# Kernel tuning notes

Hardware: AMD Instinct MI355X
Metric: run time of the kernel (lower is better)

Reference implementation:

```python
import jax, jax.numpy as jnp
import numpy as np

B, T, C = 4, 2048, 768
H, D = 12, 64          # num_heads, head_size
R = 64                 # kv_lora_rank
ROPE_THETA = 10000.0


def setup_inputs() -> dict:
    key = jax.random.key(0)
    ks = jax.random.split(key, 8)
    s = lambda fan_in: 1.0 / np.sqrt(fan_in)
    return {
        "x":      jax.random.normal(ks[0], (B, T, C), jnp.float32),
        "Wq":     jax.random.normal(ks[1], (C, H * D), jnp.float32) * s(C),
        "Wdown":  jax.random.normal(ks[2], (C, R), jnp.float32) * s(C),
        "ln_g":   jnp.ones((R,), jnp.float32),
        "ln_b":   jnp.zeros((R,), jnp.float32),
        "Wup":    jax.random.normal(ks[3], (R, 2 * H * D), jnp.float32) * s(R),
        "Wo":     jax.random.normal(ks[4], (H * D, C), jnp.float32) * s(H * D),
        "bo":     jnp.zeros((C,), jnp.float32),
    }


def _rope_cos_sin(t, d, dtype):
    # freqs over half-dim, repeated twice (rotate-half convention)
    inv_freq = 1.0 / (ROPE_THETA ** (jnp.arange(0, d, 2, dtype=jnp.float32) / d))
    ang = jnp.arange(t, dtype=jnp.float32)[:, None] * inv_freq[None, :]  # [T, D/2]
    ang = jnp.concatenate([ang, ang], axis=-1)                            # [T, D]
    return jnp.cos(ang).astype(dtype), jnp.sin(ang).astype(dtype)


def _apply_rope(q, cos, sin):
    # q: [B, H, T, D]; cos/sin: [T, D]
    d2 = q.shape[-1] // 2
    rot = jnp.concatenate([-q[..., d2:], q[..., :d2]], axis=-1)
    return q * cos + rot * sin


def reference(x, Wq, Wdown, ln_g, ln_b, Wup, Wo, bo):
    b, t, c = x.shape
    q = (x @ Wq).reshape(b, t, H, D).transpose(0, 2, 1, 3)  # [B,H,T,D]

    ckv = x @ Wdown                                         # [B,T,R]
    mu = jnp.mean(ckv, axis=-1, keepdims=True)
    var = jnp.var(ckv, axis=-1, keepdims=True)
    ckv = (ckv - mu) * jax.lax.rsqrt(var + 1e-5) * ln_g + ln_b

    kv = (ckv @ Wup).reshape(b, t, 2, H, D)
    k = kv[:, :, 0].transpose(0, 2, 1, 3)                   # [B,H,T,D]
    v = kv[:, :, 1].transpose(0, 2, 1, 3)

    cos, sin = _rope_cos_sin(t, D, x.dtype)
    q = _apply_rope(q, cos, sin)
    k = _apply_rope(k, cos, sin)

    wei = jnp.einsum("bhqd,bhkd->bhqk", q, k) * (D ** -0.5)
    causal = jnp.tril(jnp.ones((t, t), bool))
    wei = jnp.where(causal, wei, -jnp.inf)
    wei = jax.nn.softmax(wei, axis=-1)                      # dropout: eval mode (identity)

    out = jnp.einsum("bhqk,bhkd->bhqd", wei, v)             # [B,H,T,D]
    out = out.transpose(0, 2, 1, 3).reshape(b, t, H * D)
    return out @ Wo + bo
```

## Files before the change

### kernel.cpp

```cpp
#include <hip/hip_runtime.h>
#include <hip/hip_bf16.h>
#include <math.h>

#define B_ 4
#define T_ 2048
#define C_ 768
#define H_ 12
#define D_ 64
#define R_ 64
#define BT_ (B_*T_)
#define HD_ (H_*D_)

typedef __attribute__((ext_vector_type(8))) short bf16x8;
typedef __attribute__((ext_vector_type(4))) float f32x4;
typedef __attribute__((ext_vector_type(16))) float f32x16;

__device__ inline short f2bf(float f) {
  union { float f; unsigned u; } x; x.f = f;
  unsigned r = x.u + 0x7fffu + ((x.u >> 16) & 1u);
  return (short)(r >> 16);
}
__device__ inline unsigned pk_bf16(float a, float b) {
#if __has_builtin(__builtin_amdgcn_cvt_pk_bf16_f32)
  auto t = __builtin_amdgcn_cvt_pk_bf16_f32(a, b);
  unsigned u; __builtin_memcpy(&u, &t, sizeof(unsigned)); return u;
#else
  union { float f; unsigned u; } x, y; x.f = a; y.f = b;
  unsigned ra = (x.u + 0x7fffu + ((x.u >> 16) & 1u)) >> 16;
  unsigned rb = (y.u + 0x7fffu + ((y.u >> 16) & 1u)) & 0xffff0000u;
  return ra | rb;
#endif
}
__device__ inline float fexp2(float x) {
#if __has_builtin(__builtin_amdgcn_exp2f)
  return __builtin_amdgcn_exp2f(x);
#else
  return exp2f(x);
#endif
}
__device__ inline void pswap(unsigned &a, unsigned &b) {
#if __has_builtin(__builtin_amdgcn_permlane32_swap)
  auto r = __builtin_amdgcn_permlane32_swap((int)a, (int)b, false, false);
  unsigned u[2]; __builtin_memcpy(u, &r, 8);
  a = u[0]; b = u[1];
#else
  unsigned ax = __shfl_xor(a, 32), bx = __shfl_xor(b, 32);
  bool hi = (threadIdx.x & 32) != 0;
  unsigned na = hi ? bx : a;
  unsigned nb = hi ? b : ax;
  a = na; b = nb;
#endif
}
typedef __attribute__((address_space(3))) unsigned lds_u32;
typedef __attribute__((address_space(1))) const unsigned glb_u32;
__device__ inline void gload_lds16(const void* g, void* l) {
  __builtin_amdgcn_global_load_lds((glb_u32*)g, (lds_u32*)l, 16, 0, 0);
}

__device__ inline void ttile(const float* __restrict__ src, short* __restrict__ dst,
                             int K, int N, int k0, int n0, int tid, float (*tl)[33]) {
  int tx = tid & 31, ty = tid >> 5;
  #pragma unroll
  for (int r = 0; r < 4; ++r)
    tl[ty + 8 * r][tx] = src[(size_t)(k0 + ty + 8 * r) * N + n0 + tx];
  __syncthreads();
  #pragma unroll
  for (int r = 0; r < 4; ++r)
    dst[(size_t)(n0 + ty + 8 * r) * K + k0 + tx] = f2bf(tl[tx][ty + 8 * r]);
}

#define NCONV (BT_*C_/4/256)

__global__ __launch_bounds__(256) void prep_conv(
    const float* __restrict__ x, short* __restrict__ x_bf,
    const float* __restrict__ Wq, const float* __restrict__ Wd,
    const float* __restrict__ Wup, const float* __restrict__ Wo,
    short* __restrict__ W1T, short* __restrict__ WupT, short* __restrict__ WoT,
    float* __restrict__ cs, float* __restrict__ sn) {
  __shared__ float tl[32][33];
  int tid = threadIdx.x;
  if (blockIdx.x < NCONV) {
    int i = blockIdx.x * 256 + tid;
    float4 v = ((const float4*)x)[i];
    short4 o;
    o.x = f2bf(v.x); o.y = f2bf(v.y); o.z = f2bf(v.z); o.w = f2bf(v.w);
    ((short4*)x_bf)[i] = o;
    return;
  }
  int blk = blockIdx.x - NCONV;
  if (blk < 576) {
    int tk = blk % 24, tn = blk / 24;
    ttile(Wq, W1T, 768, 768, tk * 32, tn * 32, tid, tl);
  } else if (blk < 624) {
    int l = blk - 576; int tk = l % 24, tn = l / 24;
    ttile(Wd, W1T + (size_t)768 * 768, 768, 64, tk * 32, tn * 32, tid, tl);
  } else if (blk < 720) {
    int l = blk - 624; int tk = l % 2, tn = l / 2;
    ttile(Wup, WupT, 64, 1536, tk * 32, tn * 32, tid, tl);
  } else if (blk < 1296) {
    int l = blk - 720; int tk = l % 24, tn = l / 24;
    ttile(Wo, WoT, 768, 768, tk * 32, tn * 32, tid, tl);
  } else {
    int base = (blk - 1296) * 1024;
    #pragma unroll
    for (int i = 0; i < 4; ++i) {
      int idx = base + tid + i * 256;
      int j = idx & 31, t = idx >> 5;
      float invf = exp2f(-(float)j * (13.287712379549449f / 32.f));
      float a = (float)t * invf;
      cs[idx] = cosf(a);
      sn[idx] = sinf(a);
    }
  }
}

#define SC2_ 0.18033688f

template<int MODE>
__global__ __launch_bounds__(256) void gemm128(
    const short* __restrict__ A, const short* __restrict__ Bt,
    int M, int N, int K,
    float* __restrict__ out0, const float* __restrict__ bias,
    const float* __restrict__ bias2,
    short* __restrict__ ob0, short* __restrict__ ob1,
    const float* __restrict__ cs, const float* __restrict__ sn)
{
  __shared__ short SM[2 * 128 * 64];
  short* As = SM;
  short* Bs = SM + 128 * 64;
  const int m0 = blockIdx.x * 128;
  const int n0 = blockIdx.y * 128;
  const int tid = threadIdx.x, lane = tid & 63, w = tid >> 6;
  const int wr = w >> 1, wc = w & 1;
  const int fr = lane & 15, fk = (lane >> 4) * 8;
  const int rstage = lane >> 3;
  const int cstage = (lane & 7) * 8;

  f32x4 acc[4][4] = {};

  for (int k0 = 0; k0 < K; k0 += 64) {
    __syncthreads();
    #pragma unroll
    for (int i = 0; i < 4; ++i) {
      int c = w * 4 + i;
      int r = c * 8 + rstage;
      gload_lds16(&A[(size_t)(m0 + r) * K + k0 + cstage], &As[c * 512]);
      gload_lds16(&Bt[(size_t)(n0 + r) * K + k0 + cstage], &Bs[c * 512]);
    }
    __syncthreads();
    #pragma unroll
    for (int kk = 0; kk < 64; kk += 32) {
      bf16x8 a[4], b[4];
      #pragma unroll
      for (int mi = 0; mi < 4; ++mi)
        a[mi] = *(const bf16x8*)&As[(wr * 64 + mi * 16 + fr) * 64 + kk + fk];
      #pragma unroll
      for (int ni = 0; ni < 4; ++ni)
        b[ni] = *(const bf16x8*)&Bs[(wc * 64 + ni * 16 + fr) * 64 + kk + fk];
      #pragma unroll
      for (int mi = 0; mi < 4; ++mi)
        #pragma unroll
        for (int ni = 0; ni < 4; ++ni)
          acc[mi][ni] = __builtin_amdgcn_mfma_f32_16x16x32_bf16(a[mi], b[ni], acc[mi][ni], 0, 0, 0);
    }
  }

  const int er = (lane >> 4) * 4, ec = lane & 15;
  const int cb = n0 + wc * 64;

  if (cb < 768) {
    int h = cb >> 6;
    #pragma unroll
    for (int mi = 0; mi < 4; ++mi)
      #pragma unroll
      for (int r = 0; r < 4; ++r) {
        int row = m0 + wr * 64 + mi * 16 + er + r;
        int t = row & (T_ - 1), bb = row >> 11;
        short* dst = ob0 + (((size_t)(bb * H_ + h)) * T_ + t) * 64;
        #pragma unroll
        for (int ni = 0; ni < 2; ++ni) {
          int d = ni * 16 + ec;
          float c = cs[t * 32 + d], s = sn[t * 32 + d];
          if constexpr (MODE == 0) { c *= SC2_; s *= SC2_; }
          float x0 = acc[mi][ni][r], x1 = acc[mi][ni + 2][r];
          dst[d]      = f2bf(x0 * c - x1 * s);
          dst[d + 32] = f2bf(x1 * c + x0 * s);
        }
      }
  } else if constexpr (MODE == 0) {
    if (cb == 768) {
      #pragma unroll
      for (int mi = 0; mi < 4; ++mi)
        #pragma unroll
        for (int r = 0; r < 4; ++r) {
          float s = 0.f, s2 = 0.f;
          #pragma unroll
          for (int ni = 0; ni < 4; ++ni) { float v = acc[mi][ni][r]; s += v; s2 += v*v; }
          #pragma unroll
          for (int off = 1; off < 16; off <<= 1) {
            s  += __shfl_xor(s, off);
            s2 += __shfl_xor(s2, off);
          }
          float mu = s * (1.f/64.f);
          float var = s2 * (1.f/64.f) - mu * mu;
          float rstd = rsqrtf(var + 1e-5f);
          int row = m0 + wr * 64 + mi * 16 + er + r;
          #pragma unroll
          for (int ni = 0; ni < 4; ++ni) {
            int d = ni * 16 + ec;
            ob1[(size_t)row * 64 + d] = f2bf((acc[mi][ni][r] - mu) * rstd * bias[d] + bias2[d]);
          }
        }
    }
  } else {
    __syncthreads();
    short* Wl = SM + w * 2560;
    int h = (cb - 768) >> 6;
    int bb = m0 >> 11;
    int dl = lane >> 2, tl = (lane & 3) * 8;
    #pragma unroll
    for (int hp = 0; hp < 2; ++hp) {
      #pragma unroll
      for (int mi2 = 0; mi2 < 2; ++mi2) {
        int mi = hp * 2 + mi2;
        int tl0 = mi2 * 16 + er;
        #pragma unroll
        for (int ni = 0; ni < 4; ++ni) {
          int d = ni * 16 + ec;
          uint2 uu;
          uu.x = pk_bf16(acc[mi][ni][0], acc[mi][ni][1]);
          uu.y = pk_bf16(acc[mi][ni][2], acc[mi][ni][3]);
          *(uint2*)&Wl[d * 40 + tl0] = uu;
        }
      }
      int tg0 = (m0 & (T_ - 1)) + wr * 64 + hp * 32;
      #pragma unroll
      for (int j = 0; j < 4; ++j) {
        int d = j * 16 + dl;
        uint4 vv = *(const uint4*)&Wl[d * 40 + tl];
        *(uint4*)&ob1[((size_t)(bb * H_ + h) * 64 + d) * T_ + tg0 + tl] = vv;
      }
    }
  }
}

template<int MODE>
__global__ __launch_bounds__(256) void gemm64(
    const short* __restrict__ A, const short* __restrict__ Bt,
    int M, int N, int K,
    float* __restrict__ out0, const float* __restrict__ bias,
    const float* __restrict__ bias2,
    short* __restrict__ ob0, short* __restrict__ ob1,
    const float* __restrict__ cs, const float* __restrict__ sn)
{
  __shared__ short SM[128 * 64 + 64 * 64];
  short* As = SM;
  short* Bs = SM + 128 * 64;
  const int m0 = blockIdx.x * 128;
  const int n0 = blockIdx.y * 64;
  const int tid = threadIdx.x, lane = tid & 63, w = tid >> 6;
  const int fr = lane & 15, fk = (lane >> 4) * 8;
  const int rstage = lane >> 3;
  const int cstage = (lane & 7) * 8;

  f32x4 acc[2][4] = {};

  for (int k0 = 0; k0 < K; k0 += 64) {
    __syncthreads();
    #pragma unroll
    for (int i = 0; i < 4; ++i) {
      int c = w * 4 + i;
      int r = c * 8 + rstage;
      gload_lds16(&A[(size_t)(m0 + r) * K + k0 + cstage], &As[c * 512]);
    }
    #pragma unroll
    for (int i = 0; i < 2; ++i) {
      int c = w * 2 + i;
      int r = c * 8 + rstage;
      gload_lds16(&Bt[(size_t)(n0 + r) * K + k0 + cstage], &Bs[c * 512]);
    }
    __syncthreads();
    #pragma unroll
    for (int kk = 0; kk < 64; kk += 32) {
      bf16x8 a[2], b[4];
      a[0] = *(const bf16x8*)&As[(w * 32 +      fr) * 64 + kk + fk];
      a[1] = *(const bf16x8*)&As[(w * 32 + 16 + fr) * 64 + kk + fk];
      #pragma unroll
      for (int ni = 0; ni < 4; ++ni)
        b[ni] = *(const bf16x8*)&Bs[(ni * 16 + fr) * 64 + kk + fk];
      #pragma unroll
      for (int mi = 0; mi < 2; ++mi)
        #pragma unroll
        for (int ni = 0; ni < 4; ++ni)
          acc[mi][ni] = __builtin_amdgcn_mfma_f32_16x16x32_bf16(a[mi], b[ni], acc[mi][ni], 0, 0, 0);
    }
  }

  const int er = (lane >> 4) * 4, ec = lane & 15;

  if constexpr (MODE == 2) {
    #pragma unroll
    for (int mi = 0; mi < 2; ++mi)
      #pragma unroll
      for (int r = 0; r < 4; ++r) {
        int row = m0 + w * 32 + mi * 16 + er + r;
        #pragma unroll
        for (int ni = 0; ni < 4; ++ni) {
          int col = n0 + ni * 16 + ec;
          out0[(size_t)row * N + col] = acc[mi][ni][r] + bias[col];
        }
      }
    return;
  }
}

__global__ __launch_bounds__(256) void attn_mfma(
    const short* __restrict__ qgl, const short* __restrict__ kg,
    const short* __restrict__ vtg, short* __restrict__ o)
{
  __shared__ short SMa[2][2][8 * 512];

  const int bh = blockIdx.x;
  const int u  = 15 - blockIdx.y;
  const int tid = threadIdx.x, lane = tid & 63, w = tid >> 6;
  const int q32 = lane & 31, half = lane >> 5;
  const short* kb  = kg  + (size_t)bh * T_ * 64;
  const short* vtb = vtg + (size_t)bh * 64 * T_;
  const int b = bh / H_, h = bh - b * H_;

  const int wq = 4 * u + w;
  const int q0 = wq * 32;
  const int last_w = (wq >> 1) * 64;
  const int qidx = q0 + q32;
  const int kend = (2 * u + 1) * 64;

  const short* qrow = qgl + ((size_t)bh * T_ + qidx) * 64;
  bf16x8 bq[4];
  #pragma unroll
  for (int ks = 0; ks < 4; ++ks)
    bq[ks] = *(const bf16x8*)&qrow[ks * 16 + half * 8];

  f32x16 oacc[2] = {};
  float lrun = 0.f;

  auto stage = [&](int buf, int kt) {
    #pragma unroll
    for (int i = 0; i < 2; ++i) {
      int c = w * 2 + i;
      int kh = c >> 2, ks = c & 3;
      gload_lds16(kb + (size_t)(kt + kh * 32 + q32) * 64 + ks * 16 + half * 8,
                  &SMa[buf][0][c * 512]);
      gload_lds16(vtb + (size_t)(kh * 32 + q32) * T_ + kt + ks * 16 + half * 8,
                  &SMa[buf][1][c * 512]);
    }
  };

  stage(0, 0);
  __syncthreads();

  int cur = 0;
  for (int kt = 0; kt <= kend; kt += 64) {
    if (kt + 64 <= kend) stage(cur ^ 1, kt + 64);

    if (kt <= last_w) {
      const short* Kc = &SMa[cur][0][0];
      const short* Vc = &SMa[cur][1][0];
      const bool diag = (kt == last_w);
      const int dkh = diag ? (wq & 1) : 2;
      const bool skip1 = diag && ((wq & 1) == 0);

      bf16x8 bp[4];
      #pragma unroll
      for (int kh = 0; kh < 2; ++kh) {
        if (kh == 1 && skip1) break;
        f32x16 sacc = {};
        __builtin_amdgcn_s_setprio(1);
        #pragma unroll
        for (int ks = 0; ks < 4; ++ks) {
          bf16x8 a = *(const bf16x8*)&Kc[(kh * 4 + ks) * 512 + lane * 8];
          sacc = __builtin_amdgcn_mfma_f32_32x32x16_bf16(a, bq[ks], sacc, 0, 0, 0);
        }
        __builtin_amdgcn_s_setprio(0);
        float pv[16];
        if (kh != dkh) {
          #pragma unroll
          for (int r = 0; r < 16; ++r) pv[r] = fexp2(sacc[r]);
        } else {
          #pragma unroll
          for (int r = 0; r < 16; ++r) {
            int key = kt + kh * 32 + (r & 3) + 8 * (r >> 2) + 4 * half;
            pv[r] = (key <= qidx) ? fexp2(sacc[r]) : 0.f;
          }
        }
        float t0 = (pv[0] + pv[1]) + (pv[2] + pv[3]);
        float t1 = (pv[4] + pv[5]) + (pv[6] + pv[7]);
        float t2 = (pv[8] + pv[9]) + (pv[10] + pv[11]);
        float t3 = (pv[12] + pv[13]) + (pv[14] + pv[15]);
        lrun += (t0 + t1) + (t2 + t3);
        unsigned l0 = pk_bf16(pv[0],  pv[1]),  h0 = pk_bf16(pv[2],  pv[3]);
        unsigned l1 = pk_bf16(pv[4],  pv[5]),  h1 = pk_bf16(pv[6],  pv[7]);
        unsigned l2 = pk_bf16(pv[8],  pv[9]),  h2 = pk_bf16(pv[10], pv[11]);
        unsigned l3 = pk_bf16(pv[12], pv[13]), h3 = pk_bf16(pv[14], pv[15]);
        pswap(l0, l1); pswap(h0, h1);
        pswap(l2, l3); pswap(h2, h3);
        union { unsigned u[4]; bf16x8 v; } f0, f1;
        f0.u[0] = l0; f0.u[1] = h0; f0.u[2] = l1; f0.u[3] = h1;
        f1.u[0] = l2; f1.u[1] = h2; f1.u[2] = l3; f1.u[3] = h3;
        bp[2 * kh + 0] = f0.v;
        bp[2 * kh + 1] = f1.v;
      }

      __builtin_amdgcn_s_setprio(1);
      #pragma unroll
      for (int ks = 0; ks < 2; ++ks)
        #pragma unroll
        for (int dt = 0; dt < 2; ++dt) {
          bf16x8 av = *(const bf16x8*)&Vc[(dt * 4 + ks) * 512 + lane * 8];
          oacc[dt] = __builtin_amdgcn_mfma_f32_32x32x16_bf16(av, bp[ks], oacc[dt], 0, 0, 0);
        }
      if (!skip1) {
        #pragma unroll
        for (int ks = 2; ks < 4; ++ks)
          #pragma unroll
          for (int dt = 0; dt < 2; ++dt) {
            bf16x8 av = *(const bf16x8*)&Vc[(dt * 4 + ks) * 512 + lane * 8];
            oacc[dt] = __builtin_amdgcn_mfma_f32_32x32x16_bf16(av, bp[ks], oacc[dt], 0, 0, 0);
          }
      }
      __builtin_amdgcn_s_setprio(0);
    }

    __syncthreads();
    cur ^= 1;
  }

  float ltot = lrun + __shfl_xor(lrun, 32);
  float inv = 1.f / ltot;
  short* Pw = &SMa[0][0][0] + w * 2304;
  #pragma unroll
  for (int dt = 0; dt < 2; ++dt)
    #pragma unroll
    for (int g2 = 0; g2 < 4; ++g2) {
      uint2 uu;
      uu.x = pk_bf16(oacc[dt][4 * g2 + 0] * inv, oacc[dt][4 * g2 + 1] * inv);
      uu.y = pk_bf16(oacc[dt][4 * g2 + 2] * inv, oacc[dt][4 * g2 + 3] * inv);
      *(uint2*)&Pw[q32 * 72 + dt * 32 + 8 * g2 + 4 * half] = uu;
    }
  int row = lane >> 1, seg = lane & 1;
  int t = q0 + row;
  short* orow = o + ((size_t)(b * T_ + t)) * HD_ + h * 64 + seg * 32;
  #pragma unroll
  for (int i = 0; i < 4; ++i) {
    uint4 vv = *(const uint4*)&Pw[row * 72 + seg * 32 + i * 8];
    *(uint4*)&orow[i * 8] = vv;
  }
}

extern "C" void kernel_launch(void* const* d_in, const int* in_sizes, int n_in,
                              void* d_out, int out_size, void* d_ws, size_t ws_size,
                              hipStream_t stream) {
  (void)in_sizes; (void)n_in; (void)out_size; (void)ws_size;
  const float* x     = (const float*)d_in[0];
  const float* Wq    = (const float*)d_in[1];
  const float* Wdown = (const float*)d_in[2];
  const float* ln_g  = (const float*)d_in[3];
  const float* ln_b  = (const float*)d_in[4];
  const float* Wup   = (const float*)d_in[5];
  const float* Wo    = (const float*)d_in[6];
  const float* bo    = (const float*)d_in[7];
  float* out = (float*)d_out;

  char* w = (char*)d_ws;
  short* x_bf   = (short*)w;  w += (size_t)BT_ * C_    * 2;
  short* W1T    = (short*)w;  w += (size_t)896 * C_    * 2;
  short* WupT   = (short*)w;  w += (size_t)2*HD_ * R_  * 2;
  short* WoT    = (short*)w;  w += (size_t)HD_ * C_    * 2;
  short* ckv    = (short*)w;  w += (size_t)BT_ * R_    * 2;
  short* qb     = (short*)w;  w += (size_t)BT_ * HD_   * 2;
  short* kb     = (short*)w;  w += (size_t)BT_ * HD_   * 2;
  short* vt     = (short*)w;  w += (size_t)BT_ * HD_   * 2;
  short* att    = (short*)w;  w += (size_t)BT_ * HD_   * 2;
  float* cs_t   = (float*)w;  w += (size_t)T_ * 32 * 4;
  float* sn_t   = (float*)w;  w += (size_t)T_ * 32 * 4;

  prep_conv<<<NCONV + 1360, 256, 0, stream>>>(x, x_bf, Wq, Wdown, Wup, Wo,
                                              W1T, WupT, WoT, cs_t, sn_t);

  gemm128<0><<<dim3(BT_/128, 7), 256, 0, stream>>>(
      x_bf, W1T, BT_, 832, C_, nullptr, ln_g, ln_b, qb, ckv, cs_t, sn_t);

  gemm128<1><<<dim3(BT_/128, 12), 256, 0, stream>>>(
      ckv, WupT, BT_, 2*HD_, R_, nullptr, nullptr, nullptr, kb, vt, cs_t, sn_t);

  attn_mfma<<<dim3(B_*H_, 16), 256, 0, stream>>>(qb, kb, vt, att);

  gemm64<2><<<dim3(BT_/128, 12), 256, 0, stream>>>(
      att, WoT, BT_, C_, HD_, out, bo, nullptr, nullptr, nullptr, nullptr, nullptr);
}
```

Measured before the change: 193.1 us.

## Fuse x fp32-to-bf16 conversion into QKV GEMM and double-buffer GEMM K loops

Removes the separate x→bf16 conversion pass from the prep kernel. The first projection GEMM now loads fp32 x directly into registers, converts it, and writes it to LDS. That GEMM and the output-projection GEMM both get double-buffered LDS, so the next K tile loads while the current one computes. This saves a full write and read of a bf16 copy of x and hides load latency, at the cost of twice the LDS per block (64KB for gemm128 MODE0). That may lower occupancy. The latent-up GEMM (K=64) is simplified to a single stage.

New measurement: 194.4 us. About the same (+0.7%).

```diff
diff --git a/kernel.cpp b/kernel.cpp
--- a/kernel.cpp
+++ b/kernel.cpp
@@ -69,25 +69,14 @@
     dst[(size_t)(n0 + ty + 8 * r) * K + k0 + tx] = f2bf(tl[tx][ty + 8 * r]);
 }
 
-#define NCONV (BT_*C_/4/256)
-
 __global__ __launch_bounds__(256) void prep_conv(
-    const float* __restrict__ x, short* __restrict__ x_bf,
     const float* __restrict__ Wq, const float* __restrict__ Wd,
     const float* __restrict__ Wup, const float* __restrict__ Wo,
     short* __restrict__ W1T, short* __restrict__ WupT, short* __restrict__ WoT,
     float* __restrict__ cs, float* __restrict__ sn) {
   __shared__ float tl[32][33];
   int tid = threadIdx.x;
-  if (blockIdx.x < NCONV) {
-    int i = blockIdx.x * 256 + tid;
-    float4 v = ((const float4*)x)[i];
-    short4 o;
-    o.x = f2bf(v.x); o.y = f2bf(v.y); o.z = f2bf(v.z); o.w = f2bf(v.w);
-    ((short4*)x_bf)[i] = o;
-    return;
-  }
-  int blk = blockIdx.x - NCONV;
+  int blk = blockIdx.x;
   if (blk < 576) {
     int tk = blk % 24, tn = blk / 24;
     ttile(Wq, W1T, 768, 768, tk * 32, tn * 32, tid, tl);
@@ -118,16 +107,15 @@
 
 template<int MODE>
 __global__ __launch_bounds__(256) void gemm128(
-    const short* __restrict__ A, const short* __restrict__ Bt,
+    const float* __restrict__ Af, const short* __restrict__ Ab,
+    const short* __restrict__ Bt,
     int M, int N, int K,
-    float* __restrict__ out0, const float* __restrict__ bias,
-    const float* __restrict__ bias2,
+    const float* __restrict__ bias, const float* __restrict__ bias2,
     short* __restrict__ ob0, short* __restrict__ ob1,
     const float* __restrict__ cs, const float* __restrict__ sn)
 {
-  __shared__ short SM[2 * 128 * 64];
-  short* As = SM;
-  short* Bs = SM + 128 * 64;
+  constexpr int NBUF = (MODE == 0) ? 2 : 1;
+  __shared__ short SM[NBUF * 2 * 128 * 64];
   const int m0 = blockIdx.x * 128;
   const int n0 = blockIdx.y * 128;
   const int tid = threadIdx.x, lane = tid & 63, w = tid >> 6;
@@ -138,31 +126,86 @@
 
   f32x4 acc[4][4] = {};
 
-  for (int k0 = 0; k0 < K; k0 += 64) {
-    __syncthreads();
+  auto As = [&](int buf) -> short* { return SM + buf * 16384; };
+  auto Bs = [&](int buf) -> short* { return SM + buf * 16384 + 8192; };
+
+  auto compute = [&](const short* Asb, const short* Bsb) {
+    #pragma unroll
+    for (int kk = 0; kk < 64; kk += 32) {
+      bf16x8 a[4], b[4];
+      #pragma unroll
+      for (int mi = 0; mi < 4; ++mi)
+        a[mi] = *(const bf16x8*)&Asb[(wr * 64 + mi * 16 + fr) * 64 + kk + fk];
+      #pragma unroll
+      for (int ni = 0; ni < 4; ++ni)
+        b[ni] = *(const bf16x8*)&Bsb[(wc * 64 + ni * 16 + fr) * 64 + kk + fk];
+      #pragma unroll
+      for (int mi = 0; mi < 4; ++mi)
+        #pragma unroll
+        for (int ni = 0; ni < 4; ++ni)
+          acc[mi][ni] = __builtin_amdgcn_mfma_f32_16x16x32_bf16(a[mi], b[ni], acc[mi][ni], 0, 0, 0);
+    }
+  };
+
+  auto stageB = [&](short* Bsb, int k0) {
     #pragma unroll
     for (int i = 0; i < 4; ++i) {
       int c = w * 4 + i;
       int r = c * 8 + rstage;
-      gload_lds16(&A[(size_t)(m0 + r) * K + k0 + cstage], &As[c * 512]);
-      gload_lds16(&Bt[(size_t)(n0 + r) * K + k0 + cstage], &Bs[c * 512]);
-    }
+      gload_lds16(&Bt[(size_t)(n0 + r) * K + k0 + cstage], Bsb + c * 512);
+    }
+  };
+
+  if constexpr (MODE == 0) {
+    float4 fa[8];
+    auto loadA = [&](int k0) {
+      #pragma unroll
+      for (int i = 0; i < 4; ++i) {
+        int idx = tid + 256 * i;
+        int row = idx >> 3, c8 = idx & 7;
+        const float* src = Af + (size_t)(m0 + row) * 768 + k0 + c8 * 8;
+        fa[2 * i]     = *(const float4*)(src);
+        fa[2 * i + 1] = *(const float4*)(src + 4);
+      }
+    };
+    auto writeA = [&](short* Asb) {
+      #pragma unroll
+      for (int i = 0; i < 4; ++i) {
+        int idx = tid + 256 * i;
+        int row = idx >> 3, c8 = idx & 7;
+        uint4 uu;
+        uu.x = pk_bf16(fa[2 * i].x,     fa[2 * i].y);
+        uu.y = pk_bf16(fa[2 * i].z,     fa[2 * i].w);
+        uu.z = pk_bf16(fa[2 * i + 1].x, fa[2 * i + 1].y);
+        uu.w = pk_bf16(fa[2 * i + 1].z, fa[2 * i + 1].w);
+        *(uint4*)&Asb[row * 64 + c8 * 8] = uu;
+      }
+    };
+
+    loadA(0);
+    stageB(Bs(0), 0);
+    writeA(As(0));
     __syncthreads();
-    #pragma unroll
-    for (int kk = 0; kk < 64; kk += 32) {
-      bf16x8 a[4], b[4];
-      #pragma unroll
-      for (int mi = 0; mi < 4; ++mi)
-        a[mi] = *(const bf16x8*)&As[(wr * 64 + mi * 16 + fr) * 64 + kk + fk];
-      #pragma unroll
-      for (int ni = 0; ni < 4; ++ni)
-        b[ni] = *(const bf16x8*)&Bs[(wc * 64 + ni * 16 + fr) * 64 + kk + fk];
-      #pragma unroll
-      for (int mi = 0; mi < 4; ++mi)
-        #pragma unroll
-        for (int ni = 0; ni < 4; ++ni)
-          acc[mi][ni] = __builtin_amdgcn_mfma_f32_16x16x32_bf16(a[mi], b[ni], acc[mi][ni], 0, 0, 0);
-    }
+
+    int buf = 0;
+    for (int k0 = 0; k0 < K; k0 += 64) {
+      bool nxt = (k0 + 64 < K);
+      if (nxt) { loadA(k0 + 64); stageB(Bs(buf ^ 1), k0 + 64); }
+      compute(As(buf), Bs(buf));
+      if (nxt) writeA(As(buf ^ 1));
+      __syncthreads();
+      buf ^= 1;
+    }
+  } else {
+    #pragma unroll
+    for (int i = 0; i < 4; ++i) {
+      int c = w * 4 + i;
+      int r = c * 8 + rstage;
+      gload_lds16(&Ab[(size_t)(m0 + r) * K + cstage], As(0) + c * 512);
+      gload_lds16(&Bt[(size_t)(n0 + r) * K + cstage], Bs(0) + c * 512);
+    }
+    __syncthreads();
+    compute(As(0), Bs(0));
   }
 
   const int er = (lane >> 4) * 4, ec = lane & 15;
@@ -244,18 +287,12 @@
   }
 }
 
-template<int MODE>
-__global__ __launch_bounds__(256) void gemm64(
+__global__ __launch_bounds__(256) void gemm_out(
     const short* __restrict__ A, const short* __restrict__ Bt,
     int M, int N, int K,
-    float* __restrict__ out0, const float* __restrict__ bias,
-    const float* __restrict__ bias2,
-    short* __restrict__ ob0, short* __restrict__ ob1,
-    const float* __restrict__ cs, const float* __restrict__ sn)
+    float* __restrict__ out0, const float* __restrict__ bias)
 {
-  __shared__ short SM[128 * 64 + 64 * 64];
-  short* As = SM;
-  short* Bs = SM + 128 * 64;
+  __shared__ short SM[2 * (128 * 64 + 64 * 64)];
   const int m0 = blockIdx.x * 128;
   const int n0 = blockIdx.y * 64;
   const int tid = threadIdx.x, lane = tid & 63, w = tid >> 6;
@@ -265,53 +302,60 @@
 
   f32x4 acc[2][4] = {};
 
-  for (int k0 = 0; k0 < K; k0 += 64) {
-    __syncthreads();
+  auto As = [&](int buf) -> short* { return SM + buf * 12288; };
+  auto Bs = [&](int buf) -> short* { return SM + buf * 12288 + 8192; };
+
+  auto stage = [&](int buf, int k0) {
     #pragma unroll
     for (int i = 0; i < 4; ++i) {
       int c = w * 4 + i;
       int r = c * 8 + rstage;
-      gload_lds16(&A[(size_t)(m0 + r) * K + k0 + cstage], &As[c * 512]);
+      gload_lds16(&A[(size_t)(m0 + r) * K + k0 + cstage], As(buf) + c * 512);
     }
     #pragma unroll
     for (int i = 0; i < 2; ++i) {
       int c = w * 2 + i;
       int r = c * 8 + rstage;
-      gload_lds16(&Bt[(size_t)(n0 + r) * K + k0 + cstage], &Bs[c * 512]);
-    }
-    __syncthreads();
+      gload_lds16(&Bt[(size_t)(n0 + r) * K + k0 + cstage], Bs(buf) + c * 512);
+    }
+  };
+
+  stage(0, 0);
+  __syncthreads();
+
+  int buf = 0;
+  for (int k0 = 0; k0 < K; k0 += 64) {
+    if (k0 + 64 < K) stage(buf ^ 1, k0 + 64);
     #pragma unroll
     for (int kk = 0; kk < 64; kk += 32) {
       bf16x8 a[2], b[4];
-      a[0] = *(const bf16x8*)&As[(w * 32 +      fr) * 64 + kk + fk];
-      a[1] = *(const bf16x8*)&As[(w * 32 + 16 + fr) * 64 + kk + fk];
+      a[0] = *(const bf16x8*)&As(buf)[(w * 32 +      fr) * 64 + kk + fk];
+      a[1] = *(const bf16x8*)&As(buf)[(w * 32 + 16 + fr) * 64 + kk + fk];
       #pragma unroll
       for (int ni = 0; ni < 4; ++ni)
-        b[ni] = *(const bf16x8*)&Bs[(ni * 16 + fr) * 64 + kk + fk];
+        b[ni] = *(const bf16x8*)&Bs(buf)[(ni * 16 + fr) * 64 + kk + fk];
       #pragma unroll
       for (int mi = 0; mi < 2; ++mi)
         #pragma unroll
         for (int ni = 0; ni < 4; ++ni)
           acc[mi][ni] = __builtin_amdgcn_mfma_f32_16x16x32_bf16(a[mi], b[ni], acc[mi][ni], 0, 0, 0);
     }
+    __syncthreads();
+    buf ^= 1;
   }
 
   const int er = (lane >> 4) * 4, ec = lane & 15;
-
-  if constexpr (MODE == 2) {
-    #pragma unroll
-    for (int mi = 0; mi < 2; ++mi)
-      #pragma unroll
-      for (int r = 0; r < 4; ++r) {
-        int row = m0 + w * 32 + mi * 16 + er + r;
-        #pragma unroll
-        for (int ni = 0; ni < 4; ++ni) {
-          int col = n0 + ni * 16 + ec;
-          out0[(size_t)row * N + col] = acc[mi][ni][r] + bias[col];
-        }
-      }
-    return;
-  }
+  #pragma unroll
+  for (int mi = 0; mi < 2; ++mi)
+    #pragma unroll
+    for (int r = 0; r < 4; ++r) {
+      int row = m0 + w * 32 + mi * 16 + er + r;
+      #pragma unroll
+      for (int ni = 0; ni < 4; ++ni) {
+        int col = n0 + ni * 16 + ec;
+        out0[(size_t)row * N + col] = acc[mi][ni][r] + bias[col];
+      }
+    }
 }
 
 __global__ __launch_bounds__(256) void attn_mfma(
@@ -471,7 +515,6 @@
   float* out = (float*)d_out;
 
   char* w = (char*)d_ws;
-  short* x_bf   = (short*)w;  w += (size_t)BT_ * C_    * 2;
   short* W1T    = (short*)w;  w += (size_t)896 * C_    * 2;
   short* WupT   = (short*)w;  w += (size_t)2*HD_ * R_  * 2;
   short* WoT    = (short*)w;  w += (size_t)HD_ * C_    * 2;
@@ -483,17 +526,17 @@
   float* cs_t   = (float*)w;  w += (size_t)T_ * 32 * 4;
   float* sn_t   = (float*)w;  w += (size_t)T_ * 32 * 4;
 
-  prep_conv<<<NCONV + 1360, 256, 0, stream>>>(x, x_bf, Wq, Wdown, Wup, Wo,
-                                              W1T, WupT, WoT, cs_t, sn_t);
+  prep_conv<<<1360, 256, 0, stream>>>(Wq, Wdown, Wup, Wo,
+                                      W1T, WupT, WoT, cs_t, sn_t);
 
   gemm128<0><<<dim3(BT_/128, 7), 256, 0, stream>>>(
-      x_bf, W1T, BT_, 832, C_, nullptr, ln_g, ln_b, qb, ckv, cs_t, sn_t);
+      x, nullptr, W1T, BT_, 832, C_, ln_g, ln_b, qb, ckv, cs_t, sn_t);
 
   gemm128<1><<<dim3(BT_/128, 12), 256, 0, stream>>>(
-      ckv, WupT, BT_, 2*HD_, R_, nullptr, nullptr, nullptr, kb, vt, cs_t, sn_t);
+      nullptr, ckv, WupT, BT_, 2*HD_, R_, nullptr, nullptr, kb, vt, cs_t, sn_t);
 
   attn_mfma<<<dim3(B_*H_, 16), 256, 0, stream>>>(qb, kb, vt, att);
 
-  gemm64<2><<<dim3(BT_/128, 12), 256, 0, stream>>>(
-      att, WoT, BT_, C_, HD_, out, bo, nullptr, nullptr, nullptr, nullptr, nullptr);
-}
+  gemm_out<<<dim3(BT_/128, 12), 256, 0, stream>>>(
+      att, WoT, BT_, C_, HD_, out, bo);
+}
```
